# Optimization experiments

Hardware: AMD Instinct MI355X
Metric: run time of the kernel (lower is better)

The kernel has to match this reference:

```python
import jax, jax.numpy as jnp
import numpy as np
from itertools import combinations

A = 4          # anchor_points
K = 16         # neighbor_num
INTRA = A * (A - 1) // 2   # 6
CH = INTRA * 2 + A * A     # 28 = generator channels
B, N, S = 1, 8192, 4096
CIN, COUT = 64, 128


def cdist(x):
    # pairwise euclidean distances [B,N,N], zero-safe sqrt (zero grad at d=0)
    sq = jnp.sum(x * x, -1)
    d2 = sq[:, :, None] + sq[:, None, :] - 2.0 * jnp.einsum('bnc,bmc->bnm', x, x)
    d2 = jnp.maximum(d2, 0.0)
    m = d2 > 0
    return jnp.where(m, jnp.sqrt(jnp.where(m, d2, 1.0)), 0.0)


def index_points(points, idx):
    # points [B,N,...], idx [B,*] -> [B,*,...]
    return jax.vmap(lambda p, i: p[i])(points, idx)


def index_points_dists(dists, i1, i2):
    # dists [B,N,N]; result[b,...] = dists[b, i1[b,...], i2[b,...]]
    i1, i2 = jnp.broadcast_arrays(i1, i2)
    return jax.vmap(lambda d, a, b: d[a, b])(dists, i1, i2)


def generator(xyz):
    # RotationInvariantDistFea.forward(xyz, concat_raw_relative_fea=True)
    D = cdist(xyz)
    neg_nd, ni = jax.lax.top_k(-D, K)   # K >= A; smallest-K, sorted ascending
    nd = -neg_nd
    ai = ni[:, :, :A]
    # intra-anchor dists: dists to anchors 1..A-1 plus pairwise dists among them
    subs = [index_points_dists(D, ai[:, :, pi], ai[:, :, pj])[:, :, None]
            for pi, pj in combinations(range(1, A), 2)]
    intra = jnp.concatenate([nd[:, :, 1:A]] + subs, axis=2)  # [B,P,6]
    # inter-anchor dists: center anchors x neighbor anchors -> [B,P,K,A*A]
    nai = index_points(ai, ni)                                # [B,P,K,A]
    inter = index_points_dists(D, ai[:, :, None, :, None],
                               nai[:, :, :, None, :]).reshape(D.shape[0], D.shape[1], K, A * A)
    center = jnp.broadcast_to(intra[:, :, None, :], (intra.shape[0], intra.shape[1], K, INTRA))
    rf = jnp.concatenate([center, index_points(intra, ni), inter], axis=3)  # [B,P,K,28]
    return rf, ni, D


def mlp(x, W, b, g, be, act):
    # Linear + BatchNorm1d (training mode: stats over batch*points) + optional leaky_relu(0.2)
    y = x @ W + b
    mu = jnp.mean(y, (0, 1))
    var = jnp.var(y, (0, 1))
    y = (y - mu) * jax.lax.rsqrt(var + 1e-5) * g + be
    return jax.nn.leaky_relu(y, 0.2) if act else y


def forward(xyz, feature, sample_indexes, Ww, bw, gw, betaw, Wb, bb, gb, betab, Wo, bo, go, betao):
    rf_before, ni_before, D_before = generator(xyz)
    intra_before = rf_before[:, :, 0, :INTRA]
    xyz_s = index_points(xyz, sample_indexes)
    feat = index_points(feature, sample_indexes)
    intra_before = index_points(intra_before, sample_indexes)
    rf_after, ni_after, _ = generator(xyz_s)
    intra_after = rf_after[:, :, 0, :INTRA]
    a_before = index_points(ni_before[:, :, :A], sample_indexes)                  # [B,S,A]
    a_after = jax.vmap(lambda s, a: s[a])(sample_indexes, ni_after[:, :, :A])     # map to global idx
    inter = index_points_dists(D_before, a_before[:, :, :, None],
                               a_after[:, :, None, :]).reshape(B, S, A * A)
    adf = jnp.concatenate([intra_before, intra_after, inter], axis=2)             # [B,S,28]
    w = mlp(adf, Ww, bw, gw, betaw, False)
    bia = mlp(adf, Wb, bb, gb, betab, False)
    feat = jax.nn.leaky_relu(feat * w + bia, 0.2)
    feat = jnp.concatenate([feat, adf], axis=2)                                   # [B,S,92]
    feat = mlp(feat, Wo, bo, go, betao, True)                                     # [B,S,128]
    return xyz_s, feat, rf_after, ni_after


def setup_inputs():
    key = jax.random.key(0)
    ks = jax.random.split(key, 8)
    xyz = jax.random.normal(ks[0], (B, N, 3), jnp.float32)
    feature = jax.random.normal(ks[1], (B, N, CIN), jnp.float32)
    sample_indexes = jnp.stack([jax.random.permutation(jax.random.fold_in(ks[2], i), N)[:S]
                                for i in range(B)]).astype(jnp.int32)

    def lin(k, cin, cout):
        k1, k2 = jax.random.split(k)
        W = jax.random.normal(k1, (cin, cout), jnp.float32) / np.float32(np.sqrt(cin))
        b = jax.random.normal(k2, (cout,), jnp.float32) * 0.01
        return W, b, jnp.ones((cout,), jnp.float32), jnp.zeros((cout,), jnp.float32)

    Ww, bw, gw, betaw = lin(ks[5], CH, CIN)
    Wb, bb, gb, betab = lin(ks[6], CH, CIN)
    Wo, bo, go, betao = lin(ks[7], CH + CIN, COUT)
    return dict(xyz=xyz, feature=feature, sample_indexes=sample_indexes,
                Ww=Ww, bw=bw, gw=gw, betaw=betaw,
                Wb=Wb, bb=bb, gb=gb, betab=betab,
                Wo=Wo, bo=bo, go=go, betao=betao)


def reference(xyz, feature, sample_indexes, Ww, bw, gw, betaw, Wb, bb, gb, betab, Wo, bo, go, betao):
    return forward(xyz, feature, sample_indexes, Ww, bw, gw, betaw, Wb, bb, gb, betab, Wo, bo, go, betao)
```

## Files before the change

### kernel.cpp

```cpp
#include <hip/hip_runtime.h>
#include <hip/hip_bf16.h>
#include <math.h>

#define N_PTS 8192
#define S_PTS 4096
typedef unsigned long long u64;
typedef unsigned u32;

__device__ __forceinline__ float pair_dist_d(const float4 a, const float4 b) {
    double ax = a.x, ay = a.y, az = a.z;
    double bx = b.x, by = b.y, bz = b.z;
    double dx = ax - bx, dy = ay - by, dz = az - bz;
    double d2 = dx * dx + dy * dy + dz * dz;
    return d2 > 0.0 ? (float)sqrt(d2) : 0.0f;
}

__device__ __forceinline__ float d2_f32_gram(const float4 a, const float4 b) {
    float dot = __fadd_rn(__fadd_rn(__fmul_rn(a.x, b.x), __fmul_rn(a.y, b.y)),
                          __fmul_rn(a.z, b.z));
    float d2 = __fsub_rn(__fadd_rn(a.w, b.w), __fmul_rn(2.0f, dot));
    return fmaxf(d2, 0.0f);
}

__global__ __launch_bounds__(256) void stage_kernel(
        const float* __restrict__ xyz, const int* __restrict__ sidx,
        float4* __restrict__ cb, float4* __restrict__ ca,
        float* __restrict__ out_xyz_s) {
    int i = blockIdx.x * blockDim.x + threadIdx.x;
    if (i < N_PTS) {
        float x = xyz[i * 3 + 0], y = xyz[i * 3 + 1], z = xyz[i * 3 + 2];
        float sq = __fadd_rn(__fadd_rn(__fmul_rn(x, x), __fmul_rn(y, y)),
                             __fmul_rn(z, z));
        cb[i] = make_float4(x, y, z, sq);
    }
    if (i < S_PTS) {
        int si = sidx[i];
        float x = xyz[si * 3 + 0], y = xyz[si * 3 + 1], z = xyz[si * 3 + 2];
        float sq = __fadd_rn(__fadd_rn(__fmul_rn(x, x), __fmul_rn(y, y)),
                             __fmul_rn(z, z));
        ca[i] = make_float4(x, y, z, sq);
        out_xyz_s[i * 3 + 0] = x;
        out_xyz_s[i * 3 + 1] = y;
        out_xyz_s[i * 3 + 2] = z;
    }
}


template <int KOUT, int ITERS>
__device__ u64 knn_full_ladder(const float4 q, const float4* __restrict__ cand,
                               int lane) {
    u32 Lk[KOUT], Li[KOUT];
#pragma unroll
    for (int j = 0; j < KOUT; ++j) { Lk[j] = 0xFFFFFFFFu; Li[j] = 0xFFFFFFFFu; }
    int c = lane;
    for (int tt = 0; tt < ITERS; ++tt, c += 64) {
        float d2 = d2_f32_gram(q, cand[c]);
        float Df = d2 > 0.0f ? __fsqrt_rn(d2) : 0.0f;
        u32 kb = __float_as_uint(Df);
        if (kb < Lk[KOUT - 1]) {
#pragma unroll
            for (int j = KOUT - 1; j >= 1; --j) {
                bool up = kb < Lk[j - 1], ins = kb < Lk[j];
                Lk[j] = up ? Lk[j - 1] : (ins ? kb : Lk[j]);
                Li[j] = up ? Li[j - 1] : (ins ? (u32)c : Li[j]);
            }
            bool i0 = kb < Lk[0];
            Lk[0] = i0 ? kb : Lk[0];
            Li[0] = i0 ? (u32)c : Li[0];
        }
    }
    u64 Lu[KOUT];
#pragma unroll
    for (int j = 0; j < KOUT; ++j) Lu[j] = ((u64)Lk[j] << 32) | (u64)Li[j];
    u64 res = ~0ull;
#pragma unroll
    for (int r = 0; r < KOUT; ++r) {
        u64 m = Lu[0];
#pragma unroll
        for (int off = 32; off >= 1; off >>= 1) {
            u64 o = __shfl_xor(m, off, 64);
            m = (o < m) ? o : m;
        }
        if (lane == r) res = m;
        if (Lu[0] == m) {
#pragma unroll
            for (int j = 0; j < KOUT - 1; ++j) Lu[j] = Lu[j + 1];
            Lu[KOUT - 1] = ~0ull;
        }
    }
    return res;
}

template <int K, int NC>
__device__ u64 final_select(const float4 qq, const float4* __restrict__ cand,
                            const u64* bufq, u32 cnt, int lane) {
    if (cnt <= 64u) {
        u64 v = (lane < (int)cnt) ? bufq[lane] : ~0ull;
#pragma unroll
        for (int k = 2; k <= 64; k <<= 1) {
#pragma unroll
            for (int j2 = k >> 1; j2 >= 1; j2 >>= 1) {
                u64 o = __shfl_xor(v, j2, 64);
                bool keepMin = (((lane & j2) == 0) == ((lane & k) == 0));
                bool less = o < v;
                v = keepMin ? (less ? o : v) : (less ? v : o);
            }
        }
        return v;
    } else if (cnt <= 256u) {
        u64 L0 = ~0ull, L1 = ~0ull, L2 = ~0ull, L3 = ~0ull;
        for (u32 mm = lane; mm < cnt; mm += 64) {
            u64 kk = bufq[mm];
            if (kk < L3) {
                if (kk < L1) {
                    L3 = L2; L2 = L1;
                    if (kk < L0) { L1 = L0; L0 = kk; } else L1 = kk;
                } else {
                    if (kk < L2) { L3 = L2; L2 = kk; } else L3 = kk;
                }
            }
        }
        u64 res = ~0ull;
#pragma unroll
        for (int r = 0; r < K; ++r) {
            u64 mr = L0;
#pragma unroll
            for (int off = 32; off >= 1; off >>= 1) {
                u64 o = __shfl_xor(mr, off, 64);
                mr = (o < mr) ? o : mr;
            }
            if (lane == r) res = mr;
            if (L0 == mr) { L0 = L1; L1 = L2; L2 = L3; L3 = ~0ull; }
        }
        return res;
    }
    return knn_full_ladder<K, NC / 64>(qq, cand, lane);
}

template <int J, int K, int NC, int Q>
__device__ __forceinline__ u64 knn_selectq(
        const float4* qs, const float4* __restrict__ cand, int t,
        u32* mins, u64* buf, u32* shm) {
    int lane = t & 63, wid = t >> 6;
    u32 d2b[Q][J];
    u32 m[Q];
#pragma unroll
    for (int qi = 0; qi < Q; ++qi) m[qi] = 0xFFFFFFFFu;
#pragma unroll
    for (int j = 0; j < J; ++j) {
        float4 c = cand[t + 256 * j];
#pragma unroll
        for (int qi = 0; qi < Q; ++qi) {
            u32 b = __float_as_uint(d2_f32_gram(qs[qi], c));
            d2b[qi][j] = b;
            m[qi] = b < m[qi] ? b : m[qi];
        }
    }
#pragma unroll
    for (int qi = 0; qi < Q; ++qi) mins[qi * 256 + t] = m[qi];
    __syncthreads();
    if (wid < Q) {
        const u32* mq = mins + wid * 256;
        u32 v = mq[lane];
        u32 v2 = mq[lane + 64];  v = v2 < v ? v2 : v;
        v2 = mq[lane + 128];     v = v2 < v ? v2 : v;
        v2 = mq[lane + 192];     v = v2 < v ? v2 : v;
#pragma unroll
        for (int k = 2; k <= 64; k <<= 1) {
#pragma unroll
            for (int j2 = k >> 1; j2 >= 1; j2 >>= 1) {
                u32 o = __shfl_xor(v, j2, 64);
                bool keepMin = (((lane & j2) == 0) == ((lane & k) == 0));
                bool less = o < v;
                v = keepMin ? (less ? o : v) : (less ? v : o);
            }
        }
        if (lane == K - 1) shm[wid] = v;
    }
    __syncthreads();
    u32 tau[Q], c[Q], x[Q];
#pragma unroll
    for (int qi = 0; qi < Q; ++qi) {
        tau[qi] = shm[qi];
        u32 cc = 0;
#pragma unroll
        for (int j = 0; j < J; ++j) cc += (d2b[qi][j] <= tau[qi]) ? 1u : 0u;
        c[qi] = cc;
        u32 xx = cc;
#pragma unroll
        for (int off = 1; off < 64; off <<= 1) {
            u32 y = __shfl_up(xx, off, 64);
            if (lane >= off) xx += y;
        }
        x[qi] = xx;
        if (lane == 63) shm[Q + qi * 4 + wid] = xx;
    }
    __syncthreads();
    u32 cnt[Q];
#pragma unroll
    for (int qi = 0; qi < Q; ++qi) {
        u32 base = x[qi] - c[qi];
        for (int w = 0; w < wid; ++w) base += shm[Q + qi * 4 + w];
        cnt[qi] = shm[Q + qi * 4 + 0] + shm[Q + qi * 4 + 1] +
                  shm[Q + qi * 4 + 2] + shm[Q + qi * 4 + 3];
        if (cnt[qi] <= 256u) {
            u32 off = base;
#pragma unroll
            for (int j = 0; j < J; ++j) {
                if (d2b[qi][j] <= tau[qi]) {
                    float d2 = __uint_as_float(d2b[qi][j]);
                    float D = d2 > 0.0f ? __fsqrt_rn(d2) : 0.0f;
                    buf[qi * 256 + off++] = ((u64)__float_as_uint(D) << 32) |
                                            (u64)(u32)(t + 256 * j);
                }
            }
        }
    }
    __syncthreads();
    u64 res = ~0ull;
#pragma unroll
    for (int qi = 0; qi < Q; ++qi)
        if (wid == qi)
            res = final_select<K, NC>(qs[qi], cand, buf + qi * 256, cnt[qi], lane);
    return res;
}

__global__ __launch_bounds__(256, 4) void knn_kernel(
        const float4* __restrict__ cb, const float4* __restrict__ ca,
        const int* __restrict__ sidx,
        int* __restrict__ a_before, float* __restrict__ intra_before,
        int* __restrict__ ni_i, float* __restrict__ intra_after,
        float* __restrict__ out_ni) {
    __shared__ u32 mins[4 * 256];
    __shared__ u64 buf[4 * 256];
    __shared__ u32 shm[24];
    int t = threadIdx.x, lane = t & 63, wid = t >> 6;
    int bid = blockIdx.x;
    if (bid < S_PTS / 4) {
        int s0 = bid * 4;
        float4 qs[4];
#pragma unroll
        for (int qi = 0; qi < 4; ++qi) qs[qi] = ca[s0 + qi];
        u64 res = knn_selectq<16, 16, 4096, 4>(qs, ca, t, mins, buf, shm);
        if (wid < 4) {
            int s = s0 + wid;
            float4 qq = ca[s];
            int idx = (int)(res & 0xffffffffull);
            if (lane < 16) {
                ni_i[s * 16 + lane] = idx;
                out_ni[s * 16 + lane] = (float)idx;
            }
            if (lane >= 1 && lane < 4)
                intra_after[s * 6 + (lane - 1)] = pair_dist_d(qq, ca[idx]);
            int i1 = __shfl(idx, 1, 64);
            int i2 = __shfl(idx, 2, 64);
            int i3 = __shfl(idx, 3, 64);
            if (lane < 3) {
                int pa = (lane == 2) ? i2 : i1;
                int pb = (lane == 0) ? i2 : i3;
                intra_after[s * 6 + 3 + lane] = pair_dist_d(ca[pa], ca[pb]);
            }
        }
    } else {
        int s0 = (bid - S_PTS / 4) * 2;
        float4 qs[2];
        qs[0] = cb[sidx[s0]];
        qs[1] = cb[sidx[s0 + 1]];
        u64 res = knn_selectq<32, 4, 8192, 2>(qs, cb, t, mins, buf, shm);
        if (wid < 2) {
            int s = s0 + wid;
            float4 qq = cb[sidx[s]];
            int idx = (int)(res & 0xffffffffull);
            if (lane < 4) a_before[s * 4 + lane] = idx;
            if (lane >= 1 && lane < 4)
                intra_before[s * 6 + (lane - 1)] = pair_dist_d(qq, cb[idx]);
            int i1 = __shfl(idx, 1, 64);
            int i2 = __shfl(idx, 2, 64);
            int i3 = __shfl(idx, 3, 64);
            if (lane < 3) {
                int pa = (lane == 2) ? i2 : i1;
                int pb = (lane == 0) ? i2 : i3;
                intra_before[s * 6 + 3 + lane] = pair_dist_d(cb[pa], cb[pb]);
            }
        }
    }
}

__global__ __launch_bounds__(256) void assemble_kernel(
        const float4* __restrict__ ca, const float4* __restrict__ cb,
        const int* __restrict__ ni_i, const float* __restrict__ intra_after,
        const int* __restrict__ a_before, const float* __restrict__ intra_before,
        const int* __restrict__ sidx,
        float* __restrict__ out_rf, float* __restrict__ adf) {
    __shared__ int s_ni[4][16];
    __shared__ float s_rf[4][16 * 28];
    __shared__ float s_ia[4][8];
    int t = threadIdx.x, wid = t >> 6, lane = t & 63;
    int s = blockIdx.x * 4 + wid;
    if (lane < 16) s_ni[wid][lane] = ni_i[s * 16 + lane];
    if (lane < 6) s_ia[wid][lane] = intra_after[s * 6 + lane];
    __syncthreads();

    int k = lane >> 2, qq = lane & 3;
    int nai_q = ni_i[s_ni[wid][k] * 16 + qq];
    float4 pq = ca[nai_q];
#pragma unroll
    for (int p = 0; p < 4; ++p) {
        float4 pp = ca[s_ni[wid][p]];
        s_rf[wid][k * 28 + 12 + p * 4 + qq] = pair_dist_d(pp, pq);
    }
    for (int idx = lane; idx < 16 * 12; idx += 64) {
        int kk = idx / 12, c = idx % 12;
        float v = (c < 6) ? s_ia[wid][c] : intra_after[s_ni[wid][kk] * 6 + (c - 6)];
        s_rf[wid][kk * 28 + c] = v;
    }
    if (lane < 16) {
        int p = lane >> 2, q2 = lane & 3;
        int ib = a_before[s * 4 + p];
        int ia = sidx[s_ni[wid][q2]];
        adf[s * 28 + 12 + lane] = pair_dist_d(cb[ib], cb[ia]);
    } else if (lane >= 32 && lane < 38) {
        adf[s * 28 + (lane - 32)] = intra_before[s * 6 + (lane - 32)];
    } else if (lane >= 40 && lane < 46) {
        adf[s * 28 + 6 + (lane - 40)] = s_ia[wid][lane - 40];
    }
    __syncthreads();
    const int base = s * 16 * 28;
    for (int idx = lane; idx < 16 * 28; idx += 64) out_rf[base + idx] = s_rf[wid][idx];
}

__global__ __launch_bounds__(256) void mlp1_kernel(
        const float* __restrict__ adf,
        const float* __restrict__ Ww, const float* __restrict__ bw,
        const float* __restrict__ Wb, const float* __restrict__ bb,
        float* __restrict__ y_wb) {
    __shared__ float sW[28 * 128];
    __shared__ float sb[128];
    __shared__ float sA[32 * 28];
    int t = threadIdx.x;
    for (int i = t; i < 28 * 128; i += 256) {
        int k = i >> 7, c = i & 127;
        sW[i] = (c < 64) ? Ww[k * 64 + c] : Wb[k * 64 + (c - 64)];
    }
    if (t < 128) sb[t] = (t < 64) ? bw[t] : bb[t - 64];
    int s0 = blockIdx.x * 32;
    for (int i = t; i < 32 * 28; i += 256) sA[i] = adf[s0 * 28 + i];
    __syncthreads();
    int sl = t >> 3, grp = t & 7;
    int s = s0 + sl;
    float acc[16];
#pragma unroll
    for (int k = 0; k < 16; ++k) acc[k] = sb[grp * 16 + k];
    for (int k2 = 0; k2 < 28; ++k2) {
        float a = sA[sl * 28 + k2];
#pragma unroll
        for (int k = 0; k < 16; ++k)
            acc[k] = fmaf(a, sW[k2 * 128 + grp * 16 + k], acc[k]);
    }
#pragma unroll
    for (int k = 0; k < 16; ++k) y_wb[(grp * 16 + k) * 4096 + s] = acc[k];
}

__global__ __launch_bounds__(256) void stats_kernel(
        const float* __restrict__ y,
        const float* __restrict__ g0, const float* __restrict__ be0,
        const float* __restrict__ g1, const float* __restrict__ be1, int csplit,
        float* __restrict__ scale, float* __restrict__ shift) {
    int c = blockIdx.x;
    const float* p = y + c * 4096;
    float s1 = 0.0f, s2 = 0.0f;
    for (int i = threadIdx.x; i < 4096; i += 256) {
        float v = p[i];
        s1 += v;
        s2 = fmaf(v, v, s2);
    }
    __shared__ float l1[256], l2[256];
    l1[threadIdx.x] = s1;
    l2[threadIdx.x] = s2;
    __syncthreads();
    for (int off = 128; off; off >>= 1) {
        if (threadIdx.x < off) {
            l1[threadIdx.x] += l1[threadIdx.x + off];
            l2[threadIdx.x] += l2[threadIdx.x + off];
        }
        __syncthreads();
    }
    if (threadIdx.x == 0) {
        float mean = l1[0] * (1.0f / 4096.0f);
        float var = l2[0] * (1.0f / 4096.0f) - mean * mean;
        float g = (c < csplit) ? g0[c] : g1[c - csplit];
        float be = (c < csplit) ? be0[c] : be1[c - csplit];
        float sc = g / sqrtf(var + 1e-5f);
        scale[c] = sc;
        shift[c] = be - mean * sc;
    }
}

__global__ __launch_bounds__(256) void mlp2_kernel(
        const float* __restrict__ y_wb,
        const float* __restrict__ scale1, const float* __restrict__ shift1,
        const float* __restrict__ feature, const int* __restrict__ sidx,
        const float* __restrict__ adf,
        const float* __restrict__ Wo, const float* __restrict__ bo,
        float* __restrict__ y_o) {
    __shared__ float sW[92 * 128];
    __shared__ float t2[16 * 129];
    __shared__ float scat[16 * 92];
    int t = threadIdx.x;
    int s0 = blockIdx.x * 16;
    for (int i = t; i < 92 * 128; i += 256) sW[i] = Wo[i];
    for (int i = t; i < 16 * 128; i += 256) {
        int row = i & 15, c = i >> 4;
        t2[row * 129 + c] = fmaf(y_wb[c * 4096 + s0 + row], scale1[c], shift1[c]);
    }
    __syncthreads();
    for (int rr = 0; rr < 16; rr += 4) {
        int r = rr + (t >> 6);
        int c = t & 63;
        int si = sidx[s0 + r];
        float f = feature[si * 64 + c];
        float v = fmaf(f, t2[r * 129 + c], t2[r * 129 + 64 + c]);
        scat[r * 92 + c] = v >= 0.0f ? v : 0.2f * v;
    }
    for (int i = t; i < 16 * 28; i += 256) {
        int row = i / 28, k = i % 28;
        scat[row * 92 + 64 + k] = adf[(s0 + row) * 28 + k];
    }
    __syncthreads();
    int r = t >> 4, cg = t & 15;
    float acc[8];
#pragma unroll
    for (int j = 0; j < 8; ++j) acc[j] = bo[cg * 8 + j];
    for (int c = 0; c < 92; ++c) {
        float a = scat[r * 92 + c];
#pragma unroll
        for (int j = 0; j < 8; ++j)
            acc[j] = fmaf(a, sW[c * 128 + cg * 8 + j], acc[j]);
    }
    int s = s0 + r;
#pragma unroll
    for (int j = 0; j < 8; ++j) y_o[(cg * 8 + j) * 4096 + s] = acc[j];
}

__global__ __launch_bounds__(256) void final_kernel(
        const float* __restrict__ y_o,
        const float* __restrict__ scale, const float* __restrict__ shift,
        float* __restrict__ out_feat) {
    int tid = blockIdx.x * 256 + threadIdx.x;
    int j = tid >> 12;
    int s = tid & 4095;
    float v = fmaf(y_o[tid], scale[j], shift[j]);
    v = v >= 0.0f ? v : 0.2f * v;
    out_feat[s * 128 + j] = v;
}

extern "C" void kernel_launch(void* const* d_in, const int* in_sizes, int n_in,
                              void* d_out, int out_size, void* d_ws, size_t ws_size,
                              hipStream_t stream) {
    const float* xyz = (const float*)d_in[0];
    const float* feature = (const float*)d_in[1];
    const int* sidx = (const int*)d_in[2];
    const float* Ww = (const float*)d_in[3];
    const float* bw = (const float*)d_in[4];
    const float* gw = (const float*)d_in[5];
    const float* betaw = (const float*)d_in[6];
    const float* Wb = (const float*)d_in[7];
    const float* bb = (const float*)d_in[8];
    const float* gb = (const float*)d_in[9];
    const float* betab = (const float*)d_in[10];
    const float* Wo = (const float*)d_in[11];
    const float* bo = (const float*)d_in[12];
    const float* go = (const float*)d_in[13];
    const float* betao = (const float*)d_in[14];

    float* out = (float*)d_out;
    float* out_xyz = out;
    float* out_feat = out + 12288;
    float* out_rf = out + 12288 + 524288;
    float* out_ni = out + 12288 + 524288 + 1835008;

    float* ws = (float*)d_ws;
    float4* cb = (float4*)ws;
    float4* ca = (float4*)(ws + 32768);
    int* a_before = (int*)(ws + 49152);
    float* intra_before = ws + 65536;
    int* ni_i = (int*)(ws + 90112);
    float* intra_after = ws + 155648;
    float* adf = ws + 180224;
    float* y_wb = ws + 294912;
    float* y_o = ws + 819200;
    float* scale1 = ws + 1343488;
    float* shift1 = ws + 1343616;
    float* scale_o = ws + 1343744;
    float* shift_o = ws + 1343872;

    stage_kernel<<<32, 256, 0, stream>>>(xyz, sidx, cb, ca, out_xyz);
    knn_kernel<<<S_PTS / 4 + S_PTS / 2, 256, 0, stream>>>(
        cb, ca, sidx, a_before, intra_before, ni_i, intra_after, out_ni);
    assemble_kernel<<<1024, 256, 0, stream>>>(ca, cb, ni_i, intra_after, a_before,
                                              intra_before, sidx, out_rf, adf);
    mlp1_kernel<<<128, 256, 0, stream>>>(adf, Ww, bw, Wb, bb, y_wb);
    stats_kernel<<<128, 256, 0, stream>>>(y_wb, gw, betaw, gb, betab, 64, scale1, shift1);
    mlp2_kernel<<<256, 256, 0, stream>>>(y_wb, scale1, shift1, feature, sidx, adf, Wo, bo, y_o);
    stats_kernel<<<128, 256, 0, stream>>>(y_o, go, betao, go, betao, 128, scale_o, shift_o);
    final_kernel<<<2048, 256, 0, stream>>>(y_o, scale_o, shift_o, out_feat);
}
```

Baseline: 166.6 us.

## Fuse sampled and full-cloud KNN passes via permuted candidate array

Adds a perm_kernel that reorders the full point cloud so the sampled points come first, followed by the unsampled points. This lets a single KNN block compute distances once and serve both the 4096-candidate query (first 16 chunks) and the 8192-candidate query (all 32 chunks), replacing two separate block types. Candidate distances are now recomputed in a second pass and compacted with shared-memory atomics instead of being held in registers with a prefix scan. The change removes the duplicated distance work and register pressure, at the cost of an extra single-block serial kernel launch, recomputed distances and atomic contention, and a non-deterministic buffer ordering.

Result: slower. 224.0 us (+34.4%).

```diff
diff --git a/kernel.cpp b/kernel.cpp
--- a/kernel.cpp
+++ b/kernel.cpp
@@ -25,6 +25,7 @@
 __global__ __launch_bounds__(256) void stage_kernel(
         const float* __restrict__ xyz, const int* __restrict__ sidx,
         float4* __restrict__ cb, float4* __restrict__ ca,
+        float4* __restrict__ cbp, int* __restrict__ perm,
         float* __restrict__ out_xyz_s) {
     int i = blockIdx.x * blockDim.x + threadIdx.x;
     if (i < N_PTS) {
@@ -38,10 +39,51 @@
         float x = xyz[si * 3 + 0], y = xyz[si * 3 + 1], z = xyz[si * 3 + 2];
         float sq = __fadd_rn(__fadd_rn(__fmul_rn(x, x), __fmul_rn(y, y)),
                              __fmul_rn(z, z));
-        ca[i] = make_float4(x, y, z, sq);
+        float4 f4 = make_float4(x, y, z, sq);
+        ca[i] = f4;
+        cbp[i] = f4;
+        perm[i] = si;
         out_xyz_s[i * 3 + 0] = x;
         out_xyz_s[i * 3 + 1] = y;
         out_xyz_s[i * 3 + 2] = z;
+    }
+}
+
+__global__ __launch_bounds__(1024) void perm_kernel(
+        const int* __restrict__ sidx, const float4* __restrict__ cb,
+        float4* __restrict__ cbp, int* __restrict__ perm) {
+    __shared__ u64 mk[128];
+    __shared__ u32 wsum[16];
+    int t = threadIdx.x, lane = t & 63, wid = t >> 6;
+    if (t < 128) mk[t] = 0ull;
+    __syncthreads();
+    for (int i = t; i < S_PTS; i += 1024) {
+        int si = sidx[i];
+        atomicOr(&mk[si >> 6], 1ull << (si & 63));
+    }
+    __syncthreads();
+    u64 w = mk[t >> 3];
+    u32 bits = (u32)((w >> ((t & 7) * 8)) & 0xffull);
+    u32 cnt = 8u - (u32)__popc(bits);
+    u32 x = cnt;
+#pragma unroll
+    for (int off = 1; off < 64; off <<= 1) {
+        u32 y = __shfl_up(x, off, 64);
+        if (lane >= off) x += y;
+    }
+    if (lane == 63) wsum[wid] = x;
+    __syncthreads();
+    u32 base = x - cnt;
+    for (int ww = 0; ww < wid; ++ww) base += wsum[ww];
+    u32 off = (u32)S_PTS + base;
+#pragma unroll
+    for (int b = 0; b < 8; ++b) {
+        int i = t * 8 + b;
+        if (!((bits >> b) & 1u)) {
+            cbp[off] = cb[i];
+            perm[off] = i;
+            ++off;
+        }
     }
 }
 
@@ -137,151 +179,157 @@
     return knn_full_ladder<K, NC / 64>(qq, cand, lane);
 }
 
-template <int J, int K, int NC, int Q>
-__device__ __forceinline__ u64 knn_selectq(
-        const float4* qs, const float4* __restrict__ cand, int t,
-        u32* mins, u64* buf, u32* shm) {
-    int lane = t & 63, wid = t >> 6;
-    u32 d2b[Q][J];
-    u32 m[Q];
-#pragma unroll
-    for (int qi = 0; qi < Q; ++qi) m[qi] = 0xFFFFFFFFu;
-#pragma unroll
-    for (int j = 0; j < J; ++j) {
-        float4 c = cand[t + 256 * j];
-#pragma unroll
-        for (int qi = 0; qi < Q; ++qi) {
-            u32 b = __float_as_uint(d2_f32_gram(qs[qi], c));
-            d2b[qi][j] = b;
-            m[qi] = b < m[qi] ? b : m[qi];
-        }
-    }
-#pragma unroll
-    for (int qi = 0; qi < Q; ++qi) mins[qi * 256 + t] = m[qi];
-    __syncthreads();
-    if (wid < Q) {
-        const u32* mq = mins + wid * 256;
-        u32 v = mq[lane];
-        u32 v2 = mq[lane + 64];  v = v2 < v ? v2 : v;
-        v2 = mq[lane + 128];     v = v2 < v ? v2 : v;
-        v2 = mq[lane + 192];     v = v2 < v ? v2 : v;
-#pragma unroll
-        for (int k = 2; k <= 64; k <<= 1) {
-#pragma unroll
-            for (int j2 = k >> 1; j2 >= 1; j2 >>= 1) {
-                u32 o = __shfl_xor(v, j2, 64);
-                bool keepMin = (((lane & j2) == 0) == ((lane & k) == 0));
-                bool less = o < v;
-                v = keepMin ? (less ? o : v) : (less ? v : o);
-            }
-        }
-        if (lane == K - 1) shm[wid] = v;
-    }
-    __syncthreads();
-    u32 tau[Q], c[Q], x[Q];
-#pragma unroll
-    for (int qi = 0; qi < Q; ++qi) {
-        tau[qi] = shm[qi];
-        u32 cc = 0;
-#pragma unroll
-        for (int j = 0; j < J; ++j) cc += (d2b[qi][j] <= tau[qi]) ? 1u : 0u;
-        c[qi] = cc;
-        u32 xx = cc;
-#pragma unroll
-        for (int off = 1; off < 64; off <<= 1) {
-            u32 y = __shfl_up(xx, off, 64);
-            if (lane >= off) xx += y;
-        }
-        x[qi] = xx;
-        if (lane == 63) shm[Q + qi * 4 + wid] = xx;
-    }
-    __syncthreads();
-    u32 cnt[Q];
-#pragma unroll
-    for (int qi = 0; qi < Q; ++qi) {
-        u32 base = x[qi] - c[qi];
-        for (int w = 0; w < wid; ++w) base += shm[Q + qi * 4 + w];
-        cnt[qi] = shm[Q + qi * 4 + 0] + shm[Q + qi * 4 + 1] +
-                  shm[Q + qi * 4 + 2] + shm[Q + qi * 4 + 3];
-        if (cnt[qi] <= 256u) {
-            u32 off = base;
-#pragma unroll
-            for (int j = 0; j < J; ++j) {
-                if (d2b[qi][j] <= tau[qi]) {
-                    float d2 = __uint_as_float(d2b[qi][j]);
-                    float D = d2 > 0.0f ? __fsqrt_rn(d2) : 0.0f;
-                    buf[qi * 256 + off++] = ((u64)__float_as_uint(D) << 32) |
-                                            (u64)(u32)(t + 256 * j);
-                }
-            }
-        }
-    }
-    __syncthreads();
-    u64 res = ~0ull;
-#pragma unroll
-    for (int qi = 0; qi < Q; ++qi)
-        if (wid == qi)
-            res = final_select<K, NC>(qs[qi], cand, buf + qi * 256, cnt[qi], lane);
-    return res;
+__device__ __forceinline__ u32 col_tau_sort(const u32* mq, int lane) {
+    u32 v = mq[lane];
+    u32 v2 = mq[lane + 64];  v = v2 < v ? v2 : v;
+    v2 = mq[lane + 128];     v = v2 < v ? v2 : v;
+    v2 = mq[lane + 192];     v = v2 < v ? v2 : v;
+#pragma unroll
+    for (int k = 2; k <= 64; k <<= 1) {
+#pragma unroll
+        for (int j2 = k >> 1; j2 >= 1; j2 >>= 1) {
+            u32 o = __shfl_xor(v, j2, 64);
+            bool keepMin = (((lane & j2) == 0) == ((lane & k) == 0));
+            bool less = o < v;
+            v = keepMin ? (less ? o : v) : (less ? v : o);
+        }
+    }
+    return v;
 }
 
 __global__ __launch_bounds__(256, 4) void knn_kernel(
+        const float4* __restrict__ cbp, const int* __restrict__ perm,
         const float4* __restrict__ cb, const float4* __restrict__ ca,
-        const int* __restrict__ sidx,
         int* __restrict__ a_before, float* __restrict__ intra_before,
         int* __restrict__ ni_i, float* __restrict__ intra_after,
         float* __restrict__ out_ni) {
-    __shared__ u32 mins[4 * 256];
-    __shared__ u64 buf[4 * 256];
-    __shared__ u32 shm[24];
+    __shared__ u64 bufA[4 * 256];
+    __shared__ u64 bufB[4 * 256];
+    __shared__ u32 tauA[4], tauB[4], ctrA[4], ctrB[4];
     int t = threadIdx.x, lane = t & 63, wid = t >> 6;
-    int bid = blockIdx.x;
-    if (bid < S_PTS / 4) {
-        int s0 = bid * 4;
-        float4 qs[4];
-#pragma unroll
-        for (int qi = 0; qi < 4; ++qi) qs[qi] = ca[s0 + qi];
-        u64 res = knn_selectq<16, 16, 4096, 4>(qs, ca, t, mins, buf, shm);
-        if (wid < 4) {
-            int s = s0 + wid;
-            float4 qq = ca[s];
-            int idx = (int)(res & 0xffffffffull);
-            if (lane < 16) {
-                ni_i[s * 16 + lane] = idx;
-                out_ni[s * 16 + lane] = (float)idx;
+    int s0 = blockIdx.x * 4;
+    float4 qs[4];
+#pragma unroll
+    for (int qi = 0; qi < 4; ++qi) qs[qi] = ca[s0 + qi];
+
+    u32 mA[4], mB[4];
+#pragma unroll
+    for (int qi = 0; qi < 4; ++qi) { mA[qi] = 0xFFFFFFFFu; mB[qi] = 0xFFFFFFFFu; }
+#pragma unroll 8
+    for (int j = 0; j < 16; ++j) {
+        float4 c4 = cbp[t + 256 * j];
+#pragma unroll
+        for (int qi = 0; qi < 4; ++qi) {
+            u32 b = __float_as_uint(d2_f32_gram(qs[qi], c4));
+            mB[qi] = b < mB[qi] ? b : mB[qi];
+            mA[qi] = b < mA[qi] ? b : mA[qi];
+        }
+    }
+#pragma unroll 8
+    for (int j = 16; j < 32; ++j) {
+        float4 c4 = cbp[t + 256 * j];
+#pragma unroll
+        for (int qi = 0; qi < 4; ++qi) {
+            u32 b = __float_as_uint(d2_f32_gram(qs[qi], c4));
+            mB[qi] = b < mB[qi] ? b : mB[qi];
+        }
+    }
+    u32* minsA = (u32*)bufA;
+    u32* minsB = (u32*)bufB;
+#pragma unroll
+    for (int qi = 0; qi < 4; ++qi) {
+        minsA[qi * 256 + t] = mA[qi];
+        minsB[qi * 256 + t] = mB[qi];
+    }
+    __syncthreads();
+    {
+        u32 va = col_tau_sort(minsA + wid * 256, lane);
+        if (lane == 15) tauA[wid] = va;
+        u32 vb = col_tau_sort(minsB + wid * 256, lane);
+        if (lane == 3) tauB[wid] = vb;
+    }
+    if (t < 4) { ctrA[t] = 0; ctrB[t] = 0; }
+    __syncthreads();
+
+    u32 tA[4], tB[4];
+#pragma unroll
+    for (int qi = 0; qi < 4; ++qi) { tA[qi] = tauA[qi]; tB[qi] = tauB[qi]; }
+#pragma unroll 4
+    for (int j = 0; j < 16; ++j) {
+        float4 c4 = cbp[t + 256 * j];
+#pragma unroll
+        for (int qi = 0; qi < 4; ++qi) {
+            u32 b = __float_as_uint(d2_f32_gram(qs[qi], c4));
+            bool qb = b <= tB[qi];
+            bool qa = b <= tA[qi];
+            if (qb | qa) {
+                float d2 = __uint_as_float(b);
+                float D = d2 > 0.0f ? __fsqrt_rn(d2) : 0.0f;
+                u64 key = ((u64)__float_as_uint(D) << 32);
+                if (qb) {
+                    u32 o = atomicAdd(&ctrB[qi], 1u);
+                    if (o < 256u) bufB[qi * 256 + o] = key | (u32)perm[t + 256 * j];
+                }
+                if (qa) {
+                    u32 o = atomicAdd(&ctrA[qi], 1u);
+                    if (o < 256u) bufA[qi * 256 + o] = key | (u32)(t + 256 * j);
+                }
             }
-            if (lane >= 1 && lane < 4)
-                intra_after[s * 6 + (lane - 1)] = pair_dist_d(qq, ca[idx]);
-            int i1 = __shfl(idx, 1, 64);
-            int i2 = __shfl(idx, 2, 64);
-            int i3 = __shfl(idx, 3, 64);
-            if (lane < 3) {
-                int pa = (lane == 2) ? i2 : i1;
-                int pb = (lane == 0) ? i2 : i3;
-                intra_after[s * 6 + 3 + lane] = pair_dist_d(ca[pa], ca[pb]);
+        }
+    }
+#pragma unroll 4
+    for (int j = 16; j < 32; ++j) {
+        float4 c4 = cbp[t + 256 * j];
+#pragma unroll
+        for (int qi = 0; qi < 4; ++qi) {
+            u32 b = __float_as_uint(d2_f32_gram(qs[qi], c4));
+            if (b <= tB[qi]) {
+                float d2 = __uint_as_float(b);
+                float D = d2 > 0.0f ? __fsqrt_rn(d2) : 0.0f;
+                u32 o = atomicAdd(&ctrB[qi], 1u);
+                if (o < 256u)
+                    bufB[qi * 256 + o] =
+                        ((u64)__float_as_uint(D) << 32) | (u32)perm[t + 256 * j];
             }
         }
-    } else {
-        int s0 = (bid - S_PTS / 4) * 2;
-        float4 qs[2];
-        qs[0] = cb[sidx[s0]];
-        qs[1] = cb[sidx[s0 + 1]];
-        u64 res = knn_selectq<32, 4, 8192, 2>(qs, cb, t, mins, buf, shm);
-        if (wid < 2) {
-            int s = s0 + wid;
-            float4 qq = cb[sidx[s]];
-            int idx = (int)(res & 0xffffffffull);
-            if (lane < 4) a_before[s * 4 + lane] = idx;
-            if (lane >= 1 && lane < 4)
-                intra_before[s * 6 + (lane - 1)] = pair_dist_d(qq, cb[idx]);
-            int i1 = __shfl(idx, 1, 64);
-            int i2 = __shfl(idx, 2, 64);
-            int i3 = __shfl(idx, 3, 64);
-            if (lane < 3) {
-                int pa = (lane == 2) ? i2 : i1;
-                int pb = (lane == 0) ? i2 : i3;
-                intra_before[s * 6 + 3 + lane] = pair_dist_d(cb[pa], cb[pb]);
-            }
+    }
+    __syncthreads();
+
+    int s = s0 + wid;
+    float4 qq = qs[wid];
+    u32 cA = ctrA[wid], cB = ctrB[wid];
+    u64 resA = final_select<16, 4096>(qq, ca, bufA + wid * 256, cA, lane);
+    u64 resB = final_select<4, 8192>(qq, cb, bufB + wid * 256, cB, lane);
+
+    int idxA = (int)(resA & 0xffffffffull);
+    if (lane < 16) {
+        ni_i[s * 16 + lane] = idxA;
+        out_ni[s * 16 + lane] = (float)idxA;
+    }
+    if (lane >= 1 && lane < 4)
+        intra_after[s * 6 + (lane - 1)] = pair_dist_d(qq, ca[idxA]);
+    {
+        int i1 = __shfl(idxA, 1, 64);
+        int i2 = __shfl(idxA, 2, 64);
+        int i3 = __shfl(idxA, 3, 64);
+        if (lane < 3) {
+            int pa = (lane == 2) ? i2 : i1;
+            int pb = (lane == 0) ? i2 : i3;
+            intra_after[s * 6 + 3 + lane] = pair_dist_d(ca[pa], ca[pb]);
+        }
+    }
+    int idxB = (int)(resB & 0xffffffffull);
+    if (lane < 4) a_before[s * 4 + lane] = idxB;
+    if (lane >= 1 && lane < 4)
+        intra_before[s * 6 + (lane - 1)] = pair_dist_d(qq, cb[idxB]);
+    {
+        int i1 = __shfl(idxB, 1, 64);
+        int i2 = __shfl(idxB, 2, 64);
+        int i3 = __shfl(idxB, 3, 64);
+        if (lane < 3) {
+            int pa = (lane == 2) ? i2 : i1;
+            int pb = (lane == 0) ? i2 : i3;
+            intra_before[s * 6 + 3 + lane] = pair_dist_d(cb[pa], cb[pb]);
         }
     }
 }
@@ -493,10 +541,14 @@
     float* shift1 = ws + 1343616;
     float* scale_o = ws + 1343744;
     float* shift_o = ws + 1343872;
-
-    stage_kernel<<<32, 256, 0, stream>>>(xyz, sidx, cb, ca, out_xyz);
-    knn_kernel<<<S_PTS / 4 + S_PTS / 2, 256, 0, stream>>>(
-        cb, ca, sidx, a_before, intra_before, ni_i, intra_after, out_ni);
+    float4* cbp = (float4*)(ws + 1344512);
+    int* perm = (int*)(ws + 1377280);
+
+    stage_kernel<<<32, 256, 0, stream>>>(xyz, sidx, cb, ca, cbp, perm, out_xyz);
+    perm_kernel<<<1, 1024, 0, stream>>>(sidx, cb, cbp, perm);
+    knn_kernel<<<S_PTS / 4, 256, 0, stream>>>(cbp, perm, cb, ca, a_before,
+                                              intra_before, ni_i, intra_after,
+                                              out_ni);
     assemble_kernel<<<1024, 256, 0, stream>>>(ca, cb, ni_i, intra_after, a_before,
                                               intra_before, sidx, out_rf, adf);
     mlp1_kernel<<<128, 256, 0, stream>>>(adf, Ww, bw, Wb, bb, y_wb);
```
